# Kernel optimization log

Hardware: AMD Instinct MI355X
Metric: run time of the kernel (lower is better)

## Reference

```python
import jax, jax.numpy as jnp
import numpy as np

B, N, H, D, F = 32, 128, 256, 256, 512   # batch, nodes, gru hidden, latent dim, mlp hidden
SUP = 0.5                                 # ancestor_suppression_strength
EPS = 1e-6


def _gru(x, h, Wx, Wh, bx, bh):
    """torch.nn.GRUCell math; x,h: [..., H]."""
    gx = x @ Wx + bx
    gh = h @ Wh + bh
    rx, ux, nx = jnp.split(gx, 3, axis=-1)
    rh, uh, nh = jnp.split(gh, 3, axis=-1)
    r = jax.nn.sigmoid(rx + rh)
    u = jax.nn.sigmoid(ux + uh)
    n = jnp.tanh(nx + r * nh)
    return (1.0 - u) * n + u * h


def setup_inputs() -> dict:
    key = jax.random.key(0)
    ks = jax.random.split(key, 12)
    rn = lambda k, shape, fan: jax.random.normal(k, shape, jnp.float32) * (fan ** -0.5)
    return {
        "z": jax.random.normal(ks[0], (B, D), jnp.float32),
        "targets": jax.random.randint(ks[1], (B, N, N), 0, 2, jnp.int32),
        "W_init": rn(ks[2], (D, H), D),
        "b_init": jnp.zeros((H,), jnp.float32),
        "Wx": rn(ks[3], (H, 3 * H), H),
        "Wh": rn(ks[4], (H, 3 * H), H),
        "bx": jnp.zeros((3 * H,), jnp.float32),
        "bh": jnp.zeros((3 * H,), jnp.float32),
        "W1": rn(ks[5], (2 * H + D, F), 2 * H + D),
        "b1": jnp.zeros((F,), jnp.float32),
        "W2": rn(ks[6], (F, 1), F),
        "b2": jnp.zeros((1,), jnp.float32),
    }


def reference(z, targets, W_init, b_init, Wx, Wh, bx, bh, W1, b1, W2, b2):
    # teacher-forcing link targets: strictly lower-triangular (parents have smaller index)
    tgt = jnp.tril(targets.astype(jnp.float32), k=-1)  # [B,N,N]
    idx = jnp.arange(N)

    def decode_one(z1, t1):  # z1:[D], t1:[N,N]
        h0 = jnp.tanh(z1 @ W_init + b_init)                      # decoder_init: z -> node-0 state
        states0 = jnp.zeros((N, H), jnp.float32).at[0].set(h0)
        A0 = jnp.zeros((N, N), jnp.float32)                      # ancestor bitset: A[i,j]=1 iff j ancestor of i

        def step(carry, t):
            states, A, ll = carry
            m = (idx < t).astype(jnp.float32)                    # existing-node mask
            pooled = (states * m[:, None]).sum(0) / m.sum()      # mean aggregation
            h_prov = _gru(pooled, h0, Wx, Wh, bx, bh)            # provisional new-node state
            # parent logits: MLP([h_new, h_j, z]) for every existing node j
            feat = jnp.concatenate([jnp.broadcast_to(h_prov, (N, H)), states,
                                    jnp.broadcast_to(z1, (N, D))], axis=-1)   # [N, 2H+D]
            logits = (jax.nn.relu(feat @ W1 + b1) @ W2 + b2)[:, 0]            # [N]
            row = t1[t]                                          # teacher-forced parents of node t
            anc = jnp.minimum(row @ A, 1.0)                      # j already ancestor of a chosen parent
            q = jnp.clip(jax.nn.sigmoid(logits) * (1.0 - SUP * anc), EPS, 1.0 - EPS)
            ll = ll + (m * (row * jnp.log(q) + (1.0 - row) * jnp.log1p(-q))).sum()
            A = A.at[t].set(jnp.minimum(row + row @ A, 1.0))     # ancestors(t) = parents U their ancestors
            states = states.at[t].set(h_prov)
            m2 = (idx <= t).astype(jnp.float32)[:, None]
            pooled2 = (states * m2).sum(0) / m2.sum()
            upd = _gru(jnp.broadcast_to(pooled2, (N, H)), states, Wx, Wh, bx, bh)
            states = m2 * upd + (1.0 - m2) * states              # propagate info among generated nodes
            return (states, A, ll), None

        (states, A, ll), _ = jax.lax.scan(step, (states0, A0, jnp.zeros((), jnp.float32)),
                                          jnp.arange(1, N))
        return t1, ll                                            # link matrix (teacher forced), log-likelihood

    L, ll = jax.vmap(decode_one)(z, tgt)
    return L, ll
```

## Files before the change

### kernel.cpp

```cpp
#include <hip/hip_runtime.h>
#include <hip/hip_bf16.h>
#include <math.h>

#define Bz 32
#define Nn 128
#define Hh 256
#define Dd 256
#define Ff 512
#define Gg 768
#define NT 512

typedef short v8s __attribute__((ext_vector_type(8)));
typedef float f4  __attribute__((ext_vector_type(4)));
#define MFMA(a,b,c) __builtin_amdgcn_mfma_f32_16x16x32_bf16(a,b,c,0,0,0)

#define WS_H0    0
#define WS_GH0   (WS_H0 + Bz*Hh)
#define WS_ZW1   (WS_GH0 + Bz*Gg)
#define WS_XH    (WS_ZW1 + Bz*Ff)
#define WS_PSX   (WS_XH + Bz*Hh)
#define WS_LOGP  (WS_PSX + Bz*Hh)
#define WS_BAR   (WS_LOGP + Bz*8*Nn)
#define WS_XS    (WS_BAR + Bz*32)
#define WS_WB    (WS_XS + Bz*16384)
#define WS_TOTAL (WS_WB + 160*2048)

#define SM_SW    0
#define SM_SST   81920
#define SM_NLDS  147456
#define SM_PS    155648
#define SM_HPF   156672
#define SM_GX1   157696
#define SM_GX2   158080
#define SM_BASE  158464
#define SM_BXS   158720
#define SM_BHS   159104
#define SM_GH0S  159488
#define SM_ZB1S  159872
#define SM_H0S   160128
#define SM_PSN   160256
#define SM_LOGI  160384
#define SM_ROWT  160896
#define SM_AMASK 161408
#define SM_ANCW  163456
#define SM_LL    163472
#define SMEM_SZ  163488

__device__ __forceinline__ unsigned short f2bf(float x) {
  unsigned u = __float_as_uint(x);
  u = u + 0x7fffu + ((u >> 16) & 1u);
  return (unsigned short)(u >> 16);
}
__device__ __forceinline__ unsigned pack2(float e, float o) {
  return (unsigned)f2bf(e) | ((unsigned)f2bf(o) << 16);
}
__device__ __forceinline__ unsigned pkbf(float x, float y) {
  __hip_bfloat162 h = __float22bfloat162_rn(make_float2(x, y));
  union { __hip_bfloat162 h; unsigned u; } c; c.h = h; return c.u;
}
__device__ __forceinline__ float bf2f(unsigned short s) {
  return __uint_as_float(((unsigned)s) << 16);
}
__device__ __forceinline__ float sigm(float x) { return 1.0f / (1.0f + __expf(-x)); }
__device__ __forceinline__ float tanh_fast(float x) { return 2.0f / (1.0f + __expf(-2.0f*x)) - 1.0f; }
__device__ __forceinline__ v8s u4v(uint4 q) { union { uint4 q; v8s v; } c; c.q = q; return c.v; }

__device__ __forceinline__ void ast32(unsigned* p, unsigned v) {
  __hip_atomic_store(p, v, __ATOMIC_RELAXED, __HIP_MEMORY_SCOPE_AGENT);
}
__device__ __forceinline__ unsigned ald32(const unsigned* p) {
  return __hip_atomic_load(p, __ATOMIC_RELAXED, __HIP_MEMORY_SCOPE_AGENT);
}
__device__ __forceinline__ void ast64(unsigned long long* p, unsigned long long v) {
  __hip_atomic_store(p, v, __ATOMIC_RELAXED, __HIP_MEMORY_SCOPE_AGENT);
}
__device__ __forceinline__ unsigned long long ald64(const unsigned long long* p) {
  return __hip_atomic_load(p, __ATOMIC_RELAXED, __HIP_MEMORY_SCOPE_AGENT);
}

__device__ __forceinline__ void bbar(unsigned* cnt, unsigned& seq)
{
  __builtin_amdgcn_s_waitcnt(0x0F70);
  __syncthreads();
  seq += 8;
  if (threadIdx.x == 0) {
    __hip_atomic_fetch_add(cnt, 1u, __ATOMIC_RELAXED, __HIP_MEMORY_SCOPE_AGENT);
    while (__hip_atomic_load(cnt, __ATOMIC_RELAXED, __HIP_MEMORY_SCOPE_AGENT) < seq)
      __builtin_amdgcn_s_sleep(2);
  }
  __syncthreads();
}

__global__ void __launch_bounds__(256) prep_init(
    const int* __restrict__ tg, const float* __restrict__ Wx,
    const float* __restrict__ Wh, const float* __restrict__ W1,
    float* __restrict__ ws, float* __restrict__ out)
{
  const int stride = gridDim.x * blockDim.x;
  const int t0 = blockIdx.x * blockDim.x + threadIdx.x;

  for (int i = t0; i < Bz*Nn*Nn; i += stride) {
    int col = i & (Nn-1), row = (i >> 7) & (Nn-1);
    out[i] = (col < row) ? (float)tg[i] : 0.0f;
  }
  for (int i = t0; i < Bz; i += stride) out[Bz*Nn*Nn + i] = 0.0f;

  unsigned* BARu = (unsigned*)(ws + WS_BAR);
  for (int i = t0; i < Bz*32; i += stride) BARu[i] = 0u;

  unsigned* Wb = (unsigned*)(ws + WS_WB);
  for (int i = t0; i < 160*2048; i += stride) {
    int jw = i & 3, l = (i >> 2) & 63, ks = (i >> 8) & 7, nt = i >> 11;
    int k = ks*32 + (l >> 4)*8 + 2*jw;
    int n16 = l & 15;
    float lo, hi;
    if (nt < 48)       { int c = nt*16 + n16;        lo = Wh[k*Gg + c];      hi = Wh[(k+1)*Gg + c]; }
    else if (nt < 80)  { int f = (nt-48)*16 + n16;   lo = W1[(Hh+k)*Ff + f]; hi = W1[(Hh+k+1)*Ff + f]; }
    else if (nt < 128) { int c = (nt-80)*16 + n16;   lo = Wx[k*Gg + c];      hi = Wx[(k+1)*Gg + c]; }
    else               { int f = (nt-128)*16 + n16;  lo = W1[k*Ff + f];      hi = W1[(k+1)*Ff + f]; }
    Wb[i] = pack2(lo, hi);
  }
}

__global__ void __launch_bounds__(256) prep_batch(
    const float* __restrict__ z, const float* __restrict__ Wi,
    const float* __restrict__ bi, const float* __restrict__ Wh,
    const float* __restrict__ bh, const float* __restrict__ W1,
    float* __restrict__ ws)
{
  const int b = blockIdx.x, tid = threadIdx.x;
  __shared__ float zs[Dd], h0s[Hh];
  zs[tid] = z[b*Dd + tid];
  __syncthreads();
  float acc = bi[tid];
  for (int d = 0; d < Dd; ++d) acc = fmaf(zs[d], Wi[d*Hh + tid], acc);
  const float h0 = tanhf(acc);
  h0s[tid] = h0;
  ws[WS_H0 + b*Hh + tid] = h0;
  __syncthreads();
  for (int g = tid; g < Gg; g += 256) {
    float a = bh[g];
    for (int h = 0; h < Hh; ++h) a = fmaf(h0s[h], Wh[h*Gg + g], a);
    ws[WS_GH0 + b*Gg + g] = a;
  }
  for (int f = tid; f < Ff; f += 256) {
    float a = 0.0f;
    for (int d = 0; d < Dd; ++d) a = fmaf(zs[d], W1[(2*Hh + d)*Ff + f], a);
    ws[WS_ZW1 + b*Ff + f] = a;
  }
}

__device__ __forceinline__ void build_mv(const float* __restrict__ vec, int quad, v8s* av)
{
  #pragma unroll
  for (int ks = 0; ks < 8; ++ks) {
    const float4 a = *(const float4*)(vec + ks*32 + quad*8);
    const float4 c = *(const float4*)(vec + ks*32 + quad*8 + 4);
    union { unsigned u[4]; v8s v; } cv;
    cv.u[0] = pkbf(a.x, a.y); cv.u[1] = pkbf(a.z, a.w);
    cv.u[2] = pkbf(c.x, c.y); cv.u[3] = pkbf(c.z, c.w);
    av[ks] = cv.v;
  }
}
__device__ __forceinline__ void build_mv2(const float* __restrict__ va,
                                          const float* __restrict__ vb, int quad, v8s* av)
{
  #pragma unroll
  for (int ks = 0; ks < 8; ++ks) {
    const float4 a = *(const float4*)(va + ks*32 + quad*8);
    const float4 b = *(const float4*)(vb + ks*32 + quad*8);
    const float4 c = *(const float4*)(va + ks*32 + quad*8 + 4);
    const float4 d = *(const float4*)(vb + ks*32 + quad*8 + 4);
    union { unsigned u[4]; v8s v; } cv;
    cv.u[0] = pkbf(a.x+b.x, a.y+b.y); cv.u[1] = pkbf(a.z+b.z, a.w+b.w);
    cv.u[2] = pkbf(c.x+d.x, c.y+d.y); cv.u[3] = pkbf(c.z+d.z, c.w+d.w);
    av[ks] = cv.v;
  }
}

__global__ void __launch_bounds__(NT, 2) decoder_main(
    const int* __restrict__ tg,
    const float* __restrict__ bx, const float* __restrict__ bh,
    const float* __restrict__ b1, const float* __restrict__ W2,
    const float* __restrict__ b2,
    float* __restrict__ ws, float* __restrict__ out)
{
  const int blk = blockIdx.x;
  const int b = blk & 31, r = blk >> 5;
  const int tid = threadIdx.x;
  const int lane = tid & 63, wv = tid >> 6;
  const int c16 = lane & 15, quad = lane >> 4;

  extern __shared__ char smem[];
  uint4* SW4 = (uint4*)(smem + SM_SW);
  unsigned short* SST = (unsigned short*)(smem + SM_SST);
  unsigned long long* SST64 = (unsigned long long*)(smem + SM_SST);
  unsigned short* NLDS = (unsigned short*)(smem + SM_NLDS);
  unsigned* NLDSu = (unsigned*)(smem + SM_NLDS);
  unsigned long long* NLDS64 = (unsigned long long*)(smem + SM_NLDS);
  float* PS   = (float*)(smem + SM_PS);
  float* HPF  = (float*)(smem + SM_HPF);
  float* GX1  = (float*)(smem + SM_GX1);
  float* GX2  = (float*)(smem + SM_GX2);
  float* BASE = (float*)(smem + SM_BASE);
  float* BXS  = (float*)(smem + SM_BXS);
  float* BHS  = (float*)(smem + SM_BHS);
  float* GH0S = (float*)(smem + SM_GH0S);
  float* ZB1S = (float*)(smem + SM_ZB1S);
  float* H0S  = (float*)(smem + SM_H0S);
  float* PSN  = (float*)(smem + SM_PSN);
  float* LOGI = (float*)(smem + SM_LOGI);
  float* ROWT = (float*)(smem + SM_ROWT);
  unsigned* AMASK = (unsigned*)(smem + SM_AMASK);
  unsigned* ANCW = (unsigned*)(smem + SM_ANCW);
  float* LL = (float*)(smem + SM_LL);

  const float* __restrict__ h0g  = ws + WS_H0  + b*Hh;
  const float* __restrict__ gh0g = ws + WS_GH0 + b*Gg;
  const float* __restrict__ zW1g = ws + WS_ZW1 + b*Ff;
  unsigned* XHg  = (unsigned*)(ws + WS_XH) + b*Hh;
  unsigned long long* XH64 = (unsigned long long*)((unsigned*)(ws + WS_XH) + b*Hh);
  unsigned long long* PSX64 = (unsigned long long*)((unsigned*)(ws + WS_PSX) + b*Hh);
  unsigned long long* LOGP64 = (unsigned long long*)((unsigned*)(ws + WS_LOGP) + b*8*Nn);
  unsigned* LOGPg = (unsigned*)(ws + WS_LOGP) + b*8*Nn;
  unsigned* bar = (unsigned*)(ws + WS_BAR) + b*32;
  unsigned long long* XS64 = (unsigned long long*)(ws + WS_XS) + b*8192;
  const uint4* WB4 = (const uint4*)(ws + WS_WB);

  for (int i = tid; i < 16384; i += NT) ((unsigned*)SST)[i] = 0u;
  for (int i = tid; i < 5120; i += NT) {
    const int lt = i >> 9, q = i & 511;
    int gt;
    if (lt < 6) { const int gate = lt >> 1, tt = lt & 1; gt = gate*16 + 2*r + tt; }
    else        { gt = 48 + 4*r + (lt - 6); }
    SW4[lt*512 + q] = WB4[gt*512 + q];
  }
  if (tid < Hh) PS[tid] = h0g[tid];
  if (tid < 32) H0S[tid] = h0g[32*r + tid];
  if (tid < 96) {
    const int g = tid >> 5, hcl = tid & 31;
    const int col = g*256 + 32*r + hcl;
    BXS[tid] = bx[col]; BHS[tid] = bh[col]; GH0S[tid] = gh0g[col];
  }
  if (tid >= 96 && tid < 160) { const int f = 64*r + (tid - 96); ZB1S[tid-96] = zW1g[f] + b1[f]; }
  if (tid == 160) *LL = 0.0f;
  for (int i = tid; i < Nn*4; i += NT) AMASK[i] = 0u;
  float w2r[4];
  #pragma unroll
  for (int ft = 0; ft < 4; ++ft) w2r[ft] = W2[64*r + ft*16 + c16];
  const float b2v = b2[0];
  unsigned bseq = 0;
  __syncthreads();
  if (tid < Hh) {
    const int c = tid;
    SST[(c>>5)*512 + ((c>>3)&3)*128 + (c&7)] = f2bf(PS[c]);
  }
  __syncthreads();

  for (int t = 1; t < Nn; ++t) {
    const float invt  = 1.0f / (float)t;
    const float invt1 = 1.0f / (float)(t + 1);
    const int Mtot = (t + 16) >> 4;
    const int Mlog = (t + 15) >> 4;
    const int mtc = t >> 4;

    if (wv < 6) {
      v8s av[8]; build_mv(PS, quad, av);
      const int g = wv >> 1, tt = wv & 1;
      const uint4* Bp = WB4 + (80 + g*16 + 2*r + tt)*512 + lane;
      f4 c = {0.0f,0.0f,0.0f,0.0f};
      #pragma unroll
      for (int ks = 0; ks < 8; ++ks) c = MFMA(av[ks], u4v(Bp[ks*64]), c);
      if (quad == 0) GX1[g*32 + tt*16 + c16] = c[0];
    }
    __syncthreads();
    if (tid < 32) {
      const int hcl = tid;
      const float gxr = GX1[hcl]*invt    + BXS[hcl];
      const float gxu = GX1[32+hcl]*invt + BXS[32+hcl];
      const float gxn = GX1[64+hcl]*invt + BXS[64+hcl];
      const float rv = sigm(gxr + GH0S[hcl]);
      const float uv = sigm(gxu + GH0S[32+hcl]);
      const float nv = tanh_fast(gxn + rv*GH0S[64+hcl]);
      ast32(XHg + 32*r + hcl, __float_as_uint((1.0f-uv)*nv + uv*H0S[hcl]));
    }
    bbar(bar, bseq);

    if (tid < 128) {
      const unsigned long long v = ald64(XH64 + tid);
      HPF[2*tid]   = __uint_as_float((unsigned)v);
      HPF[2*tid+1] = __uint_as_float((unsigned)(v >> 32));
    }
    if (tid < 256) NLDSu[mtc*256 + tid] = 0u;
    else if (tid < 384) {
      const int j = tid - 256;
      ROWT[j] = (r == 0 && j < t) ? (float)tg[b*Nn*Nn + t*Nn + j] : 0.0f;
      LOGI[j] = 0.0f;
    } else if (tid < 416) PSN[tid - 384] = 0.0f;
    else if (tid < 420) ANCW[tid - 416] = 0u;
    __syncthreads();

    if (tid < Hh) {
      const int c = tid;
      SST[(mtc*8 + (c>>5))*512 + (((c>>3)&3)*16 + (t&15))*8 + (c&7)] = f2bf(HPF[c]);
    }
    for (int j = wv; j < 10; j += 8) {
      if (j < 6) {
        v8s av[8]; build_mv2(PS, HPF, quad, av);
        const int g = j >> 1, tt = j & 1;
        const uint4* Bp = WB4 + (80 + g*16 + 2*r + tt)*512 + lane;
        f4 c = {0.0f,0.0f,0.0f,0.0f};
        #pragma unroll
        for (int ks = 0; ks < 8; ++ks) c = MFMA(av[ks], u4v(Bp[ks*64]), c);
        if (quad == 0) GX2[g*32 + tt*16 + c16] = c[0]*invt1 + BXS[g*32 + tt*16 + c16];
      } else {
        v8s av[8]; build_mv(HPF, quad, av);
        const int ft = j - 6;
        const uint4* Bp = WB4 + (128 + 4*r + ft)*512 + lane;
        f4 c = {0.0f,0.0f,0.0f,0.0f};
        #pragma unroll
        for (int ks = 0; ks < 8; ++ks) c = MFMA(av[ks], u4v(Bp[ks*64]), c);
        if (quad == 0) BASE[ft*16 + c16] = c[0] + ZB1S[ft*16 + c16];
      }
    }
    if (r == 0 && tid < Nn && tid < t && ROWT[tid] > 0.5f) {
      atomicOr(&ANCW[0], AMASK[tid*4+0]); atomicOr(&ANCW[1], AMASK[tid*4+1]);
      atomicOr(&ANCW[2], AMASK[tid*4+2]); atomicOr(&ANCW[3], AMASK[tid*4+3]);
    }
    __syncthreads();

    const int njobs = Mtot + Mlog;
    for (int j = wv; j < njobs; j += 8) {
      const int isG = (j < Mtot);
      const int mt = isG ? j : (j - Mtot);
      v8s af[8];
      #pragma unroll
      for (int ks = 0; ks < 8; ++ks)
        af[ks] = *(const v8s*)(SST + (mt*8 + ks)*512 + lane*8);
      if (isG) {
        f4 cr0={0,0,0,0}, cr1={0,0,0,0}, cu0={0,0,0,0}, cu1={0,0,0,0}, cn0={0,0,0,0}, cn1={0,0,0,0};
        #pragma unroll
        for (int ks = 0; ks < 8; ++ks) {
          cr0 = MFMA(af[ks], u4v(SW4[(0*8 + ks)*64 + lane]), cr0);
          cr1 = MFMA(af[ks], u4v(SW4[(1*8 + ks)*64 + lane]), cr1);
          cu0 = MFMA(af[ks], u4v(SW4[(2*8 + ks)*64 + lane]), cu0);
          cu1 = MFMA(af[ks], u4v(SW4[(3*8 + ks)*64 + lane]), cu1);
          cn0 = MFMA(af[ks], u4v(SW4[(4*8 + ks)*64 + lane]), cn0);
          cn1 = MFMA(af[ks], u4v(SW4[(5*8 + ks)*64 + lane]), cn1);
        }
        #pragma unroll
        for (int ct = 0; ct < 2; ++ct) {
          const int hcl = ct*16 + c16;
          const f4 cr = ct ? cr1 : cr0;
          const f4 cu = ct ? cu1 : cu0;
          const f4 cn = ct ? cn1 : cn0;
          const float gxr = GX2[hcl], gxu = GX2[32+hcl], gxn = GX2[64+hcl];
          const float bhr = BHS[hcl], bhu = BHS[32+hcl], bhn = BHS[64+hcl];
          float colsum = 0.0f;
          #pragma unroll
          for (int rg = 0; rg < 4; ++rg) {
            const int row = mt*16 + quad*4 + rg;
            if (row <= t) {
              const int spi = ((hcl>>3)*16 + quad*4 + rg)*8 + (hcl & 7);
              const float old = bf2f(SST[(mt*8 + r)*512 + spi]);
              const float rv = sigm(gxr + cr[rg] + bhr);
              const float uv = sigm(gxu + cu[rg] + bhu);
              const float nv = tanh_fast(gxn + rv*(cn[rg] + bhn));
              const float ns = (1.0f-uv)*nv + uv*old;
              NLDS[mt*512 + spi] = f2bf(ns);
              colsum += ns;
            }
          }
          colsum += __shfl_down(colsum, 16);
          colsum += __shfl_down(colsum, 32);
          if (lane < 16) atomicAdd(&PSN[ct*16 + lane], colsum);
        }
      } else {
        f4 cl0={0,0,0,0}, cl1={0,0,0,0}, cl2={0,0,0,0}, cl3={0,0,0,0};
        #pragma unroll
        for (int ks = 0; ks < 8; ++ks) {
          cl0 = MFMA(af[ks], u4v(SW4[(6*8 + ks)*64 + lane]), cl0);
          cl1 = MFMA(af[ks], u4v(SW4[(7*8 + ks)*64 + lane]), cl1);
          cl2 = MFMA(af[ks], u4v(SW4[(8*8 + ks)*64 + lane]), cl2);
          cl3 = MFMA(af[ks], u4v(SW4[(9*8 + ks)*64 + lane]), cl3);
        }
        #pragma unroll
        for (int rg = 0; rg < 4; ++rg) {
          float v = fmaxf(cl0[rg] + BASE[c16],    0.0f)*w2r[0]
                  + fmaxf(cl1[rg] + BASE[16+c16], 0.0f)*w2r[1]
                  + fmaxf(cl2[rg] + BASE[32+c16], 0.0f)*w2r[2]
                  + fmaxf(cl3[rg] + BASE[48+c16], 0.0f)*w2r[3];
          v += __shfl_xor(v, 1); v += __shfl_xor(v, 2);
          v += __shfl_xor(v, 4); v += __shfl_xor(v, 8);
          const int row = mt*16 + quad*4 + rg;
          if (c16 == 0 && row < t) atomicAdd(&LOGI[row], v);
        }
      }
    }
    __syncthreads();

    for (int i = tid; i < Mtot*128; i += NT) {
      const int mt = i >> 7, q = i & 127;
      const unsigned long long v = NLDS64[i];
      ast64(XS64 + (mt*8 + r)*128 + q, v);
      SST64[(mt*8 + r)*128 + q] = v;
    }
    if (tid < 64) ast64(LOGP64 + r*64 + tid, ((const unsigned long long*)LOGI)[tid]);
    else if (tid < 80) ast64(PSX64 + r*16 + (tid - 64), ((const unsigned long long*)PSN)[tid - 64]);
    bbar(bar, bseq);

    for (int i = tid; i < Mtot*1024; i += NT) {
      const int ks = (i >> 7) & 7;
      if (ks != r) SST64[i] = ald64(XS64 + i);
    }
    if (tid < 128) {
      const unsigned long long v = ald64(PSX64 + tid);
      PS[2*tid]   = __uint_as_float((unsigned)v);
      PS[2*tid+1] = __uint_as_float((unsigned)(v >> 32));
    }
    if (r == 0) {
      float term = 0.0f;
      if (tid < t) {
        float lsum = b2v;
        #pragma unroll
        for (int rr = 0; rr < 8; ++rr)
          lsum += __uint_as_float(ald32(LOGPg + rr*Nn + tid));
        const float anc = (float)((ANCW[tid >> 5] >> (tid & 31)) & 1u);
        float q = sigm(lsum) * (1.0f - 0.5f*anc);
        q = fminf(fmaxf(q, 1e-6f), 1.0f - 1e-6f);
        term = ROWT[tid]*logf(q) + (1.0f - ROWT[tid])*log1pf(-q);
      }
      if (wv < 2) {
        #pragma unroll
        for (int off = 32; off; off >>= 1) term += __shfl_down(term, off);
        if (lane == 0) atomicAdd(LL, term);
        const unsigned long long bal = __ballot(tid < t && ROWT[tid] > 0.5f);
        if (lane == 0) {
          AMASK[t*4 + 2*wv]     = (unsigned)bal         | ANCW[2*wv];
          AMASK[t*4 + 2*wv + 1] = (unsigned)(bal >> 32) | ANCW[2*wv + 1];
        }
      }
    }
    __syncthreads();
  }

  if (r == 0 && tid == 0) out[Bz*Nn*Nn + b] = *LL;
}

extern "C" void kernel_launch(void* const* d_in, const int* in_sizes, int n_in,
                              void* d_out, int out_size, void* d_ws, size_t ws_size,
                              hipStream_t stream)
{
  const float* z  = (const float*)d_in[0];
  const int*   tg = (const int*)  d_in[1];
  const float* Wi = (const float*)d_in[2];
  const float* bi = (const float*)d_in[3];
  const float* Wx = (const float*)d_in[4];
  const float* Wh = (const float*)d_in[5];
  const float* bx = (const float*)d_in[6];
  const float* bh = (const float*)d_in[7];
  const float* W1 = (const float*)d_in[8];
  const float* b1 = (const float*)d_in[9];
  const float* W2 = (const float*)d_in[10];
  const float* b2 = (const float*)d_in[11];
  float* out = (float*)d_out;
  float* ws  = (float*)d_ws;

  hipFuncSetAttribute((const void*)decoder_main,
                      hipFuncAttributeMaxDynamicSharedMemorySize, SMEM_SZ);

  hipLaunchKernelGGL(prep_init, dim3(512), dim3(256), 0, stream, tg, Wx, Wh, W1, ws, out);
  hipLaunchKernelGGL(prep_batch, dim3(Bz), dim3(256), 0, stream, z, Wi, bi, Wh, bh, W1, ws);

  void* args[] = { (void*)&tg, (void*)&bx, (void*)&bh, (void*)&b1,
                   (void*)&W2, (void*)&b2, (void*)&ws, (void*)&out };
  hipLaunchCooperativeKernel((void*)decoder_main, dim3(256), dim3(NT),
                             args, SMEM_SZ, stream);
}
```

Before: 2.065 ms.

## Split grid barrier into signal/wait and overlap GRU/MLP MFMAs with barrier latency

Splits the inter-block barrier into a signal phase and a wait phase. The GRU and MLP matmuls over the already-finalized state tiles now run between signal and wait, so the cross-block barrier latency is hidden; only the newest tile is computed after the barrier. Each wave now owns a fixed pair of tiles with accumulators held in registers. Ancestor masks and target rows are computed redundantly in every block, and the log-likelihood reduction rotates across blocks with atomics to global output. This raises register pressure with 12 accumulators and assumes the output slot is zeroed beforehand.

```diff
diff --git a/kernel.cpp b/kernel.cpp
--- a/kernel.cpp
+++ b/kernel.cpp
@@ -43,7 +43,6 @@
 #define SM_ROWT  160896
 #define SM_AMASK 161408
 #define SM_ANCW  163456
-#define SM_LL    163472
 #define SMEM_SZ  163488
 
 __device__ __forceinline__ unsigned short f2bf(float x) {
@@ -78,13 +77,17 @@
   return __hip_atomic_load(p, __ATOMIC_RELAXED, __HIP_MEMORY_SCOPE_AGENT);
 }
 
-__device__ __forceinline__ void bbar(unsigned* cnt, unsigned& seq)
+__device__ __forceinline__ void bsig(unsigned* cnt)
 {
   __builtin_amdgcn_s_waitcnt(0x0F70);
   __syncthreads();
+  if (threadIdx.x == 0)
+    __hip_atomic_fetch_add(cnt, 1u, __ATOMIC_RELAXED, __HIP_MEMORY_SCOPE_AGENT);
+}
+__device__ __forceinline__ void bwait(unsigned* cnt, unsigned& seq)
+{
   seq += 8;
   if (threadIdx.x == 0) {
-    __hip_atomic_fetch_add(cnt, 1u, __ATOMIC_RELAXED, __HIP_MEMORY_SCOPE_AGENT);
     while (__hip_atomic_load(cnt, __ATOMIC_RELAXED, __HIP_MEMORY_SCOPE_AGENT) < seq)
       __builtin_amdgcn_s_sleep(2);
   }
@@ -175,6 +178,40 @@
     cv.u[0] = pkbf(a.x+b.x, a.y+b.y); cv.u[1] = pkbf(a.z+b.z, a.w+b.w);
     cv.u[2] = pkbf(c.x+d.x, c.y+d.y); cv.u[3] = pkbf(c.z+d.z, c.w+d.w);
     av[ks] = cv.v;
+  }
+}
+
+__device__ __forceinline__ void gemm_gru_pair(
+    const unsigned short* SST, const uint4* SW4, int lane,
+    int mt0, bool do0, int mt1, bool do1, f4* acc)
+{
+  v8s a0[8], a1[8];
+  if (do0) {
+    #pragma unroll
+    for (int ks = 0; ks < 8; ++ks) a0[ks] = *(const v8s*)(SST + (mt0*8 + ks)*512 + lane*8);
+  }
+  if (do1) {
+    #pragma unroll
+    for (int ks = 0; ks < 8; ++ks) a1[ks] = *(const v8s*)(SST + (mt1*8 + ks)*512 + lane*8);
+  }
+  #pragma unroll
+  for (int ks = 0; ks < 8; ++ks) {
+    const v8s b0 = u4v(SW4[(0*8 + ks)*64 + lane]);
+    const v8s b1 = u4v(SW4[(1*8 + ks)*64 + lane]);
+    const v8s b2 = u4v(SW4[(2*8 + ks)*64 + lane]);
+    const v8s b3 = u4v(SW4[(3*8 + ks)*64 + lane]);
+    const v8s b4 = u4v(SW4[(4*8 + ks)*64 + lane]);
+    const v8s b5 = u4v(SW4[(5*8 + ks)*64 + lane]);
+    if (do0) {
+      acc[0] = MFMA(a0[ks], b0, acc[0]); acc[1] = MFMA(a0[ks], b1, acc[1]);
+      acc[2] = MFMA(a0[ks], b2, acc[2]); acc[3] = MFMA(a0[ks], b3, acc[3]);
+      acc[4] = MFMA(a0[ks], b4, acc[4]); acc[5] = MFMA(a0[ks], b5, acc[5]);
+    }
+    if (do1) {
+      acc[6] = MFMA(a1[ks], b0, acc[6]); acc[7]  = MFMA(a1[ks], b1, acc[7]);
+      acc[8] = MFMA(a1[ks], b2, acc[8]); acc[9]  = MFMA(a1[ks], b3, acc[9]);
+      acc[10]= MFMA(a1[ks], b4, acc[10]); acc[11]= MFMA(a1[ks], b5, acc[11]);
+    }
   }
 }
 
@@ -213,7 +250,6 @@
   float* ROWT = (float*)(smem + SM_ROWT);
   unsigned* AMASK = (unsigned*)(smem + SM_AMASK);
   unsigned* ANCW = (unsigned*)(smem + SM_ANCW);
-  float* LL = (float*)(smem + SM_LL);
 
   const float* __restrict__ h0g  = ws + WS_H0  + b*Hh;
   const float* __restrict__ gh0g = ws + WS_GH0 + b*Gg;
@@ -243,7 +279,6 @@
     BXS[tid] = bx[col]; BHS[tid] = bh[col]; GH0S[tid] = gh0g[col];
   }
   if (tid >= 96 && tid < 160) { const int f = 64*r + (tid - 96); ZB1S[tid-96] = zW1g[f] + b1[f]; }
-  if (tid == 160) *LL = 0.0f;
   for (int i = tid; i < Nn*4; i += NT) AMASK[i] = 0u;
   float w2r[4];
   #pragma unroll
@@ -262,7 +297,7 @@
     const float invt1 = 1.0f / (float)(t + 1);
     const int Mtot = (t + 16) >> 4;
     const int Mlog = (t + 15) >> 4;
-    const int mtc = t >> 4;
+    const int mtc = Mtot - 1;
 
     if (wv < 6) {
       v8s av[8]; build_mv(PS, quad, av);
@@ -272,8 +307,15 @@
       #pragma unroll
       for (int ks = 0; ks < 8; ++ks) c = MFMA(av[ks], u4v(Bp[ks*64]), c);
       if (quad == 0) GX1[g*32 + tt*16 + c16] = c[0];
+    } else {
+      const int j = tid - 384;
+      ROWT[j] = (j < t) ? (float)tg[b*Nn*Nn + t*Nn + j] : 0.0f;
+      LOGI[j] = 0.0f;
+      if (j < 32) PSN[j] = 0.0f;
+      if (j < 4) ANCW[j] = 0u;
     }
     __syncthreads();
+
     if (tid < 32) {
       const int hcl = tid;
       const float gxr = GX1[hcl]*invt    + BXS[hcl];
@@ -284,25 +326,68 @@
       const float nv = tanh_fast(gxn + rv*GH0S[64+hcl]);
       ast32(XHg + 32*r + hcl, __float_as_uint((1.0f-uv)*nv + uv*H0S[hcl]));
     }
-    bbar(bar, bseq);
+    if (tid < Nn && tid < t && ROWT[tid] > 0.5f) {
+      atomicOr(&ANCW[0], AMASK[tid*4+0]); atomicOr(&ANCW[1], AMASK[tid*4+1]);
+      atomicOr(&ANCW[2], AMASK[tid*4+2]); atomicOr(&ANCW[3], AMASK[tid*4+3]);
+    }
+    bsig(bar);
+
+    f4 acc[12];
+    #pragma unroll
+    for (int i = 0; i < 12; ++i) acc[i] = (f4){0.0f,0.0f,0.0f,0.0f};
+    const bool isGRU = (wv < 4);
+    const int mt0 = isGRU ? 2*wv : 2*(wv - 4);
+    const int mt1 = mt0 + 1;
+    if (isGRU) {
+      gemm_gru_pair(SST, SW4, lane, mt0, mt0 < mtc, mt1, mt1 < mtc, acc);
+    } else {
+      const bool do0 = (mt0 < Mlog), do1 = (mt1 < Mlog);
+      v8s a0[8], a1[8];
+      if (do0) {
+        #pragma unroll
+        for (int ks = 0; ks < 8; ++ks) a0[ks] = *(const v8s*)(SST + (mt0*8 + ks)*512 + lane*8);
+      }
+      if (do1) {
+        #pragma unroll
+        for (int ks = 0; ks < 8; ++ks) a1[ks] = *(const v8s*)(SST + (mt1*8 + ks)*512 + lane*8);
+      }
+      #pragma unroll
+      for (int ks = 0; ks < 8; ++ks) {
+        const v8s c0 = u4v(SW4[(6*8 + ks)*64 + lane]);
+        const v8s c1 = u4v(SW4[(7*8 + ks)*64 + lane]);
+        const v8s c2 = u4v(SW4[(8*8 + ks)*64 + lane]);
+        const v8s c3 = u4v(SW4[(9*8 + ks)*64 + lane]);
+        if (do0) {
+          acc[0] = MFMA(a0[ks], c0, acc[0]); acc[1] = MFMA(a0[ks], c1, acc[1]);
+          acc[2] = MFMA(a0[ks], c2, acc[2]); acc[3] = MFMA(a0[ks], c3, acc[3]);
+        }
+        if (do1) {
+          acc[4] = MFMA(a1[ks], c0, acc[4]); acc[5] = MFMA(a1[ks], c1, acc[5]);
+          acc[6] = MFMA(a1[ks], c2, acc[6]); acc[7] = MFMA(a1[ks], c3, acc[7]);
+        }
+      }
+    }
+    bwait(bar, bseq);
 
     if (tid < 128) {
       const unsigned long long v = ald64(XH64 + tid);
       HPF[2*tid]   = __uint_as_float((unsigned)v);
       HPF[2*tid+1] = __uint_as_float((unsigned)(v >> 32));
     }
-    if (tid < 256) NLDSu[mtc*256 + tid] = 0u;
-    else if (tid < 384) {
-      const int j = tid - 256;
-      ROWT[j] = (r == 0 && j < t) ? (float)tg[b*Nn*Nn + t*Nn + j] : 0.0f;
-      LOGI[j] = 0.0f;
-    } else if (tid < 416) PSN[tid - 384] = 0.0f;
-    else if (tid < 420) ANCW[tid - 416] = 0u;
     __syncthreads();
 
-    if (tid < Hh) {
+    if (tid < 256) {
       const int c = tid;
       SST[(mtc*8 + (c>>5))*512 + (((c>>3)&3)*16 + (t&15))*8 + (c&7)] = f2bf(HPF[c]);
+    } else if (tid < 512) {
+      NLDSu[mtc*256 + (tid - 256)] = 0u;
+    }
+    if (wv < 2) {
+      const unsigned long long bal = __ballot(tid < t && ROWT[tid] > 0.5f);
+      if (lane == 0) {
+        AMASK[t*4 + 2*wv]     = (unsigned)bal         | ANCW[2*wv];
+        AMASK[t*4 + 2*wv + 1] = (unsigned)(bal >> 32) | ANCW[2*wv + 1];
+      }
     }
     for (int j = wv; j < 10; j += 8) {
       if (j < 6) {
@@ -323,77 +408,62 @@
         if (quad == 0) BASE[ft*16 + c16] = c[0] + ZB1S[ft*16 + c16];
       }
     }
-    if (r == 0 && tid < Nn && tid < t && ROWT[tid] > 0.5f) {
-      atomicOr(&ANCW[0], AMASK[tid*4+0]); atomicOr(&ANCW[1], AMASK[tid*4+1]);
-      atomicOr(&ANCW[2], AMASK[tid*4+2]); atomicOr(&ANCW[3], AMASK[tid*4+3]);
-    }
     __syncthreads();
 
-    const int njobs = Mtot + Mlog;
-    for (int j = wv; j < njobs; j += 8) {
-      const int isG = (j < Mtot);
-      const int mt = isG ? j : (j - Mtot);
-      v8s af[8];
+    if (isGRU && wv == (mtc >> 1)) {
+      gemm_gru_pair(SST, SW4, lane, mt0, mtc == mt0, mt1, mtc == mt1, acc);
+    }
+
+    if (isGRU) {
       #pragma unroll
-      for (int ks = 0; ks < 8; ++ks)
-        af[ks] = *(const v8s*)(SST + (mt*8 + ks)*512 + lane*8);
-      if (isG) {
-        f4 cr0={0,0,0,0}, cr1={0,0,0,0}, cu0={0,0,0,0}, cu1={0,0,0,0}, cn0={0,0,0,0}, cn1={0,0,0,0};
-        #pragma unroll
-        for (int ks = 0; ks < 8; ++ks) {
-          cr0 = MFMA(af[ks], u4v(SW4[(0*8 + ks)*64 + lane]), cr0);
-          cr1 = MFMA(af[ks], u4v(SW4[(1*8 + ks)*64 + lane]), cr1);
-          cu0 = MFMA(af[ks], u4v(SW4[(2*8 + ks)*64 + lane]), cu0);
-          cu1 = MFMA(af[ks], u4v(SW4[(3*8 + ks)*64 + lane]), cu1);
-          cn0 = MFMA(af[ks], u4v(SW4[(4*8 + ks)*64 + lane]), cn0);
-          cn1 = MFMA(af[ks], u4v(SW4[(5*8 + ks)*64 + lane]), cn1);
+      for (int s = 0; s < 2; ++s) {
+        const int mt = s ? mt1 : mt0;
+        if (mt < Mtot) {
+          const f4* ac = acc + 6*s;
+          #pragma unroll
+          for (int ct = 0; ct < 2; ++ct) {
+            const int hcl = ct*16 + c16;
+            const f4 cr = ac[0 + ct], cu = ac[2 + ct], cn = ac[4 + ct];
+            const float gxr = GX2[hcl], gxu = GX2[32+hcl], gxn = GX2[64+hcl];
+            const float bhr = BHS[hcl], bhu = BHS[32+hcl], bhn = BHS[64+hcl];
+            float colsum = 0.0f;
+            #pragma unroll
+            for (int rg = 0; rg < 4; ++rg) {
+              const int row = mt*16 + quad*4 + rg;
+              if (row <= t) {
+                const int spi = ((hcl>>3)*16 + quad*4 + rg)*8 + (hcl & 7);
+                const float old = bf2f(SST[(mt*8 + r)*512 + spi]);
+                const float rv = sigm(gxr + cr[rg] + bhr);
+                const float uv = sigm(gxu + cu[rg] + bhu);
+                const float nv = tanh_fast(gxn + rv*(cn[rg] + bhn));
+                const float ns = (1.0f-uv)*nv + uv*old;
+                NLDS[mt*512 + spi] = f2bf(ns);
+                colsum += ns;
+              }
+            }
+            colsum += __shfl_down(colsum, 16);
+            colsum += __shfl_down(colsum, 32);
+            if (lane < 16) atomicAdd(&PSN[ct*16 + lane], colsum);
+          }
         }
-        #pragma unroll
-        for (int ct = 0; ct < 2; ++ct) {
-          const int hcl = ct*16 + c16;
-          const f4 cr = ct ? cr1 : cr0;
-          const f4 cu = ct ? cu1 : cu0;
-          const f4 cn = ct ? cn1 : cn0;
-          const float gxr = GX2[hcl], gxu = GX2[32+hcl], gxn = GX2[64+hcl];
-          const float bhr = BHS[hcl], bhu = BHS[32+hcl], bhn = BHS[64+hcl];
-          float colsum = 0.0f;
+      }
+    } else {
+      #pragma unroll
+      for (int s = 0; s < 2; ++s) {
+        const int mt = s ? mt1 : mt0;
+        if (mt < Mlog) {
+          const f4* ac = acc + 4*s;
           #pragma unroll
           for (int rg = 0; rg < 4; ++rg) {
+            float v = fmaxf(ac[0][rg] + BASE[c16],    0.0f)*w2r[0]
+                    + fmaxf(ac[1][rg] + BASE[16+c16], 0.0f)*w2r[1]
+                    + fmaxf(ac[2][rg] + BASE[32+c16], 0.0f)*w2r[2]
+                    + fmaxf(ac[3][rg] + BASE[48+c16], 0.0f)*w2r[3];
+            v += __shfl_xor(v, 1); v += __shfl_xor(v, 2);
+            v += __shfl_xor(v, 4); v += __shfl_xor(v, 8);
             const int row = mt*16 + quad*4 + rg;
-            if (row <= t) {
-              const int spi = ((hcl>>3)*16 + quad*4 + rg)*8 + (hcl & 7);
-              const float old = bf2f(SST[(mt*8 + r)*512 + spi]);
-              const float rv = sigm(gxr + cr[rg] + bhr);
-              const float uv = sigm(gxu + cu[rg] + bhu);
-              const float nv = tanh_fast(gxn + rv*(cn[rg] + bhn));
-              const float ns = (1.0f-uv)*nv + uv*old;
-              NLDS[mt*512 + spi] = f2bf(ns);
-              colsum += ns;
-            }
+            if (c16 == 0 && row < t) atomicAdd(&LOGI[row], v);
           }
-          colsum += __shfl_down(colsum, 16);
-          colsum += __shfl_down(colsum, 32);
-          if (lane < 16) atomicAdd(&PSN[ct*16 + lane], colsum);
-        }
-      } else {
-        f4 cl0={0,0,0,0}, cl1={0,0,0,0}, cl2={0,0,0,0}, cl3={0,0,0,0};
-        #pragma unroll
-        for (int ks = 0; ks < 8; ++ks) {
-          cl0 = MFMA(af[ks], u4v(SW4[(6*8 + ks)*64 + lane]), cl0);
-          cl1 = MFMA(af[ks], u4v(SW4[(7*8 + ks)*64 + lane]), cl1);
-          cl2 = MFMA(af[ks], u4v(SW4[(8*8 + ks)*64 + lane]), cl2);
-          cl3 = MFMA(af[ks], u4v(SW4[(9*8 + ks)*64 + lane]), cl3);
-        }
-        #pragma unroll
-        for (int rg = 0; rg < 4; ++rg) {
-          float v = fmaxf(cl0[rg] + BASE[c16],    0.0f)*w2r[0]
-                  + fmaxf(cl1[rg] + BASE[16+c16], 0.0f)*w2r[1]
-                  + fmaxf(cl2[rg] + BASE[32+c16], 0.0f)*w2r[2]
-                  + fmaxf(cl3[rg] + BASE[48+c16], 0.0f)*w2r[3];
-          v += __shfl_xor(v, 1); v += __shfl_xor(v, 2);
-          v += __shfl_xor(v, 4); v += __shfl_xor(v, 8);
-          const int row = mt*16 + quad*4 + rg;
-          if (c16 == 0 && row < t) atomicAdd(&LOGI[row], v);
         }
       }
     }
@@ -407,7 +477,8 @@
     }
     if (tid < 64) ast64(LOGP64 + r*64 + tid, ((const unsigned long long*)LOGI)[tid]);
     else if (tid < 80) ast64(PSX64 + r*16 + (tid - 64), ((const unsigned long long*)PSN)[tid - 64]);
-    bbar(bar, bseq);
+    bsig(bar);
+    bwait(bar, bseq);
 
     for (int i = tid; i < Mtot*1024; i += NT) {
       const int ks = (i >> 7) & 7;
@@ -418,7 +489,7 @@
       PS[2*tid]   = __uint_as_float((unsigned)v);
       PS[2*tid+1] = __uint_as_float((unsigned)(v >> 32));
     }
-    if (r == 0) {
+    if (r == (t & 7)) {
       float term = 0.0f;
       if (tid < t) {
         float lsum = b2v;
@@ -433,18 +504,11 @@
       if (wv < 2) {
         #pragma unroll
         for (int off = 32; off; off >>= 1) term += __shfl_down(term, off);
-        if (lane == 0) atomicAdd(LL, term);
-        const unsigned long long bal = __ballot(tid < t && ROWT[tid] > 0.5f);
-        if (lane == 0) {
-          AMASK[t*4 + 2*wv]     = (unsigned)bal         | ANCW[2*wv];
-          AMASK[t*4 + 2*wv + 1] = (unsigned)(bal >> 32) | ANCW[2*wv + 1];
-        }
+        if (lane == 0) atomicAdd(&out[Bz*Nn*Nn + b], term);
       }
     }
     __syncthreads();
   }
-
-  if (r == 0 && tid == 0) out[Bz*Nn*Nn + b] = *LL;
 }
 
 extern "C" void kernel_launch(void* const* d_in, const int* in_sizes, int n_in,
```

Result: slower. 2.859 ms (+38.5%).
